# Optimization experiments

Measured on AMD Instinct MI355X. Metric: run time of the kernel, lower is better.

## Reference

```python
import jax, jax.numpy as jnp
import numpy as np

DIM = 512
HEADS = 8
DIM_HEAD = 64
INNER = HEADS * DIM_HEAD  # 512
B, N = 32, 512
LN_EPS = 1e-5


def setup_inputs() -> dict:
    key = jax.random.key(0)
    ks = jax.random.split(key, 8)
    inp = {
        "q": jax.random.normal(ks[0], (B, N, DIM), jnp.float32),
        "k": jax.random.normal(ks[1], (B, N, DIM), jnp.float32),
        "v": jax.random.normal(ks[2], (B, N, DIM), jnp.float32),
        "ln_w": jnp.ones((DIM,), jnp.float32),
        "ln_b": jnp.zeros((DIM,), jnp.float32),
        "W_in": jax.random.normal(ks[3], (DIM, INNER), jnp.float32) / np.sqrt(DIM),
        "W_out": jax.random.normal(ks[4], (INNER, DIM), jnp.float32) / np.sqrt(INNER),
        "b_out": jnp.zeros((DIM,), jnp.float32),
        "cov_w_raw": jnp.float32(0.6),
        "var_w_raw": jnp.float32(0.2),
    }
    return inp


def _project(x, ln_w, ln_b, W_in):
    # LayerNorm(dim) -> Linear(dim, inner, bias=False) -> 'b n (h d) -> h b n d'
    mu = jnp.mean(x, axis=-1, keepdims=True)
    var = jnp.var(x, axis=-1, keepdims=True)  # biased, as in nn.LayerNorm
    xn = (x - mu) / jnp.sqrt(var + LN_EPS) * ln_w + ln_b
    f = xn @ W_in  # [B, N, inner]
    Bq, Nq, _ = f.shape
    f = f.reshape(Bq, Nq, HEADS, DIM_HEAD)
    return jnp.transpose(f, (2, 0, 1, 3))  # [h, B, N, d]


def reference(q, k, v, ln_w, ln_b, W_in, W_out, b_out, cov_w_raw, var_w_raw):
    f_q = _project(q, ln_w, ln_b, W_in)  # [h, B, N, d]
    f_k = _project(k, ln_w, ln_b, W_in)
    f_v = _project(v, ln_w, ln_b, W_in)

    d = f_q.shape[-1]

    # cosine similarity: (q . k) / (||q|| ||k||)
    dots = jnp.einsum('hbnd,hbmd->hbnm', f_q, f_k)
    qn = jnp.linalg.norm(f_q, axis=-1)  # [h, B, N]
    kn = jnp.linalg.norm(f_k, axis=-1)  # [h, B, M]
    cosine_sim = dots / (qn[..., :, None] * kn[..., None, :])

    # basic covariance component: centered dot / d
    qc = f_q - jnp.mean(f_q, axis=-1, keepdims=True)
    kc = f_k - jnp.mean(f_k, axis=-1, keepdims=True)
    cov_component = jnp.einsum('hbnd,hbmd->hbnm', qc, kc) / d

    # variance component: outer product of per-token variances (unbiased) / d
    q_var = jnp.var(f_q, axis=-1, ddof=1)  # [h, B, N]
    k_var = jnp.var(f_k, axis=-1, ddof=1)  # [h, B, M]
    var_component = (q_var[..., :, None] * k_var[..., None, :]) / d

    cov_w = jax.nn.sigmoid(cov_w_raw)
    var_w = jax.nn.sigmoid(var_w_raw)
    cos_w = 1.0 - cov_w - var_w

    scores = cos_w * cosine_sim + cov_w * cov_component + var_w * var_component
    out = jnp.einsum('hbnm,hbmd->hbnd', scores, f_v)  # no softmax in cosine variant

    # 'h b n d -> b n (h d)'
    out = jnp.transpose(out, (1, 2, 0, 3)).reshape(out.shape[1], out.shape[2], INNER)
    return out @ W_out + b_out
```

## Files before the change

kernel.cpp:

```cpp
#include <hip/hip_runtime.h>
#include <stdint.h>

using u16 = unsigned short;
using u32 = unsigned int;
using bf16x8 = __bf16 __attribute__((ext_vector_type(8)));
using f32x4  = float __attribute__((ext_vector_type(4)));

__device__ __forceinline__ float bflo(u32 u){ return __uint_as_float(u << 16); }
__device__ __forceinline__ float bfhi(u32 u){ return __uint_as_float(u & 0xffff0000u); }
__device__ __forceinline__ u16 f2bf(float f){
  u32 u = __float_as_uint(f);
  u += 0x7fffu + ((u >> 16) & 1u);
  return (u16)(u >> 16);
}
__device__ __forceinline__ u32 pk2(float a, float b){
  return (u32)f2bf(a) | ((u32)f2bf(b) << 16);
}
__device__ __forceinline__ void gload16(const void* g, void* l){
  __builtin_amdgcn_global_load_lds(
      (const __attribute__((address_space(1))) void*)(uintptr_t)(g),
      (__attribute__((address_space(3))) void*)(uintptr_t)(l), 16, 0, 0);
}

__global__ __launch_bounds__(256) void prepcast_k(
    const float* __restrict__ q, const float* __restrict__ k, const float* __restrict__ v,
    const float* __restrict__ lnw, const float* __restrict__ lnb,
    u16* __restrict__ xnq, u16* __restrict__ xnk, u16* __restrict__ xnv,
    const float* __restrict__ Win, const float* __restrict__ Wout,
    u16* __restrict__ WinT, u16* __restrict__ WoutT){
  __shared__ float tile[32][33];
  if (blockIdx.x >= 12288){
    int bi = blockIdx.x - 12288;
    int bz = bi >> 8; bi &= 255;
    int bx = bi & 15, by = bi >> 4;
    const float* src = bz ? Wout : Win;
    u16* dst = bz ? WoutT : WinT;
    int tx = threadIdx.x & 31, ty = threadIdx.x >> 5;
    int c0 = bx * 32, r0 = by * 32;
#pragma unroll
    for (int i = 0; i < 4; ++i)
      tile[ty + i*8][tx] = src[(size_t)(r0 + ty + i*8)*512 + c0 + tx];
    __syncthreads();
#pragma unroll
    for (int i = 0; i < 4; ++i)
      dst[(size_t)(c0 + ty + i*8)*512 + r0 + tx] = f2bf(tile[tx][ty + i*8]);
    return;
  }
  int row = blockIdx.x * 4 + (threadIdx.x >> 6);
  int l = threadIdx.x & 63;
  const float* x = (row < 16384) ? q : (row < 32768) ? k : v;
  u16* xo = (row < 16384) ? xnq : (row < 32768) ? xnk : xnv;
  int r = row & 16383;
  const float* rp = x + (size_t)r * 512 + l*8;
  float4 a = *(const float4*)rp, c = *(const float4*)(rp + 4);
  float sum = ((a.x+a.y)+(a.z+a.w)) + ((c.x+c.y)+(c.z+c.w));
  float ss  = ((a.x*a.x+a.y*a.y)+(a.z*a.z+a.w*a.w)) + ((c.x*c.x+c.y*c.y)+(c.z*c.z+c.w*c.w));
#pragma unroll
  for (int off = 32; off; off >>= 1){
    sum += __shfl_xor(sum, off);
    ss  += __shfl_xor(ss,  off);
  }
  float mu = sum * (1.f/512.f);
  float rs = rsqrtf(ss * (1.f/512.f) - mu*mu + 1e-5f);
  float4 w0 = *(const float4*)(lnw + l*8), w1 = *(const float4*)(lnw + l*8 + 4);
  float4 b0 = *(const float4*)(lnb + l*8), b1 = *(const float4*)(lnb + l*8 + 4);
  uint4 pk;
  pk.x = pk2((a.x-mu)*rs*w0.x + b0.x, (a.y-mu)*rs*w0.y + b0.y);
  pk.y = pk2((a.z-mu)*rs*w0.z + b0.z, (a.w-mu)*rs*w0.w + b0.w);
  pk.z = pk2((c.x-mu)*rs*w1.x + b1.x, (c.y-mu)*rs*w1.y + b1.y);
  pk.w = pk2((c.z-mu)*rs*w1.z + b1.z, (c.w-mu)*rs*w1.w + b1.w);
  *(uint4*)((char*)xo + (size_t)r*1024 + l*16) = pk;
}

template<int MAP, int FSTAT>
__device__ __forceinline__ void gemm_body(
    const u16* __restrict__ A, const u16* __restrict__ B,
    u16* __restrict__ C, float* __restrict__ stat, int ldC, int bid,
    char* sA, char* sB){
  const int t = threadIdx.x, w = t >> 6, l = t & 63;
  const int wr = w >> 1, wc = w & 1;
  const int lr = l & 15, lg = l >> 4;
  int bx, by;
  if (MAP == 0){ bx = bid & 127; by = bid >> 7; }
  else { int j = bid >> 3; bx = j & 3; by = (bid & 7) + 8*(j >> 2); }
  const int row0 = bx * 128, col0 = by * 128;
  f32x4 acc[4][4] = {};

  const int sc = t >> 3, k8 = t & 7;
  const int sso = (k8*16) ^ ((sc & 7) << 4);
  const char* Ap = (const char*)A + ((size_t)(row0 + sc) << 10) + sso;
  const char* Bp = (const char*)B + ((size_t)(col0 + sc) << 10) + sso;

  for (int kt = 0; kt < 8; ++kt){
    __syncthreads();
#pragma unroll
    for (int ii = 0; ii < 4; ++ii){
      gload16(Ap + (size_t)ii*32768 + kt*128, sA + ii*4096 + w*1024);
      gload16(Bp + (size_t)ii*32768 + kt*128, sB + ii*4096 + w*1024);
    }
    __syncthreads();
#pragma unroll
    for (int kk = 0; kk < 2; ++kk){
      bf16x8 af[4], bfg[4];
#pragma unroll
      for (int m = 0; m < 4; ++m){
        int r = wr*64 + m*16 + lr;
        af[m] = *(const bf16x8*)(sA + r*128 + ((kk*64 + lg*16) ^ ((r & 7) << 4)));
      }
#pragma unroll
      for (int n = 0; n < 4; ++n){
        int r = wc*64 + n*16 + lr;
        bfg[n] = *(const bf16x8*)(sB + r*128 + ((kk*64 + lg*16) ^ ((r & 7) << 4)));
      }
#pragma unroll
      for (int m = 0; m < 4; ++m)
#pragma unroll
        for (int n = 0; n < 4; ++n)
          acc[m][n] = __builtin_amdgcn_mfma_f32_16x16x32_bf16(af[m], bfg[n], acc[m][n], 0, 0, 0);
    }
  }
  float cs[4] = {}, cs2[4] = {};
#pragma unroll
  for (int m = 0; m < 4; ++m){
#pragma unroll
    for (int q = 0; q < 4; ++q){
      int ri = wr*64 + m*16 + lg*4 + q;
      float fv[4];
#pragma unroll
      for (int n = 0; n < 4; ++n){
        int ci = wc*64 + n*16 + lr;
        fv[n] = acc[m][n][q];
        C[(size_t)(row0 + ri)*ldC + (col0 + ci)] = f2bf(fv[n]);
        if (FSTAT == 2){ cs[n] += fv[n]; cs2[n] += fv[n]*fv[n]; }
      }
      if (FSTAT == 1){
        float s  = (fv[0]+fv[1]) + (fv[2]+fv[3]);
        float s2 = (fv[0]*fv[0]+fv[1]*fv[1]) + (fv[2]*fv[2]+fv[3]*fv[3]);
#pragma unroll
        for (int off = 1; off < 16; off <<= 1){ s += __shfl_xor(s, off); s2 += __shfl_xor(s2, off); }
        if (lr == 0){
          int head = (col0 >> 6) + wc;
          *(float2*)(stat + ((size_t)(row0 + ri)*8 + head)*2) = make_float2(s, s2);
        }
      }
    }
  }
  if (FSTAT == 2){
    int head = (row0 >> 6) + wr;
#pragma unroll
    for (int n = 0; n < 4; ++n){
      float s = cs[n], s2 = cs2[n];
      s += __shfl_xor(s, 16); s2 += __shfl_xor(s2, 16);
      s += __shfl_xor(s, 32); s2 += __shfl_xor(s2, 32);
      if (lg == 0){
        int tok = col0 + wc*64 + n*16 + lr;
        *(float2*)(stat + ((size_t)tok*8 + head)*2) = make_float2(s, s2);
      }
    }
  }
}

__global__ __launch_bounds__(256) void proj_k(
    const u16* __restrict__ xnq, const u16* __restrict__ xnk, const u16* __restrict__ xnv,
    const u16* __restrict__ Wt,
    u16* __restrict__ fq, u16* __restrict__ kT, u16* __restrict__ vT,
    float* __restrict__ qstat, float* __restrict__ kstat){
  __shared__ __align__(16) char sA[16384];
  __shared__ __align__(16) char sB[16384];
  int bid = blockIdx.x;
  if (bid < 512)
    gemm_body<0,1>(xnq, Wt, fq, qstat, 512, bid, sA, sB);
  else if (bid < 1024)
    gemm_body<1,2>(Wt, xnk, kT, kstat, 16384, bid - 512, sA, sB);
  else
    gemm_body<1,0>(Wt, xnv, vT, nullptr, 16384, bid - 1024, sA, sB);
}

__global__ __launch_bounds__(256) void outgemm_k(
    const u16* __restrict__ A, const u16* __restrict__ B,
    float* __restrict__ Cf, const float* __restrict__ bias){
  __shared__ __align__(16) char sA[16384];
  __shared__ __align__(16) char sB[16384];
  const int t = threadIdx.x, w = t >> 6, l = t & 63;
  const int wr = w >> 1, wc = w & 1;
  const int lr = l & 15, lg = l >> 4;
  const int row0 = blockIdx.x * 128, col0 = blockIdx.y * 128;
  f32x4 acc[4][4] = {};

  const int sc = t >> 3, k8 = t & 7;
  const int sso = (k8*16) ^ ((sc & 7) << 4);
  const char* Ap = (const char*)A + ((size_t)(row0 + sc) << 10) + sso;
  const char* Bp = (const char*)B + ((size_t)(col0 + sc) << 10) + sso;

  for (int kt = 0; kt < 8; ++kt){
    __syncthreads();
#pragma unroll
    for (int ii = 0; ii < 4; ++ii){
      gload16(Ap + (size_t)ii*32768 + kt*128, sA + ii*4096 + w*1024);
      gload16(Bp + (size_t)ii*32768 + kt*128, sB + ii*4096 + w*1024);
    }
    __syncthreads();
#pragma unroll
    for (int kk = 0; kk < 2; ++kk){
      bf16x8 af[4], bfg[4];
#pragma unroll
      for (int m = 0; m < 4; ++m){
        int r = wr*64 + m*16 + lr;
        af[m] = *(const bf16x8*)(sA + r*128 + ((kk*64 + lg*16) ^ ((r & 7) << 4)));
      }
#pragma unroll
      for (int n = 0; n < 4; ++n){
        int r = wc*64 + n*16 + lr;
        bfg[n] = *(const bf16x8*)(sB + r*128 + ((kk*64 + lg*16) ^ ((r & 7) << 4)));
      }
#pragma unroll
      for (int m = 0; m < 4; ++m)
#pragma unroll
        for (int n = 0; n < 4; ++n)
          acc[m][n] = __builtin_amdgcn_mfma_f32_16x16x32_bf16(af[m], bfg[n], acc[m][n], 0, 0, 0);
    }
  }
#pragma unroll
  for (int m = 0; m < 4; ++m){
#pragma unroll
    for (int q = 0; q < 4; ++q){
      int r = row0 + wr*64 + m*16 + lg*4 + q;
#pragma unroll
      for (int n = 0; n < 4; ++n){
        int cc = col0 + wc*64 + n*16 + lr;
        Cf[(size_t)r*512 + cc] = acc[m][n][q] + bias[cc];
      }
    }
  }
}

__global__ __launch_bounds__(512) void attn_k(
    const u16* __restrict__ fq, const u16* __restrict__ kT, const u16* __restrict__ vT,
    const float* __restrict__ qstat, const float* __restrict__ kstat,
    u16* __restrict__ ao,
    const float* __restrict__ cwr, const float* __restrict__ vwr){
  __shared__ __align__(16) char smem[131072 + 1664*4];
  float* sStat = (float*)(smem + 131072);
  float* sS1 = sStat + 1536;
  float* sS2 = sStat + 1600;

  const int t = threadIdx.x, w = t >> 6, l = t & 63;
  const int lr = l & 15, lg = l >> 4;
  const int h = blockIdx.x & 7, b = blockIdx.x >> 3;

  float cwv = 1.f/(1.f + __expf(-*cwr));
  float vwv = 1.f/(1.f + __expf(-*vwr));
  float cosw = 1.f - cwv - vwv;

  const char* kTb = (const char*)kT + (size_t)h*64*32768 + (size_t)b*1024;
  const char* vTb = (const char*)vT + (size_t)h*64*32768 + (size_t)b*1024;
#pragma unroll
  for (int ii = 0; ii < 8; ++ii){
    int c = ii*512 + t, d = c >> 6, u = c & 63;
    int so = d*32768 + ((u ^ (d & 7)) << 4);
    gload16(kTb + so, smem + ii*8192 + w*1024);
    gload16(vTb + so, smem + 65536 + ii*8192 + w*1024);
  }
  {
    float2 ksr = *(const float2*)(kstat + ((size_t)(b*512 + t)*8 + h)*2);
    float mk = ksr.x * (1.f/64.f);
    sStat[t]        = rsqrtf(ksr.y);
    sStat[512 + t]  = mk;
    sStat[1024 + t] = (ksr.y - 64.f*mk*mk) * (1.f/63.f);
  }
  __syncthreads();

  const int jt = (w >> 1), itp = (w & 1);
  f32x4 m2acc[2] = {}, m1acc[2] = {};
  {
    const int j = jt*16 + lr;
#pragma unroll
    for (int ks = 0; ks < 16; ++ks){
      int u = ks*4 + lg;
      bf16x8 af = *(const bf16x8*)(smem + 65536 + j*1024 + ((u ^ (j & 7)) << 4));
#pragma unroll
      for (int tt = 0; tt < 2; ++tt){
        int i = (itp*2 + tt)*16 + lr;
        bf16x8 bf = *(const bf16x8*)(smem + i*1024 + ((u ^ (i & 7)) << 4));
        m2acc[tt] = __builtin_amdgcn_mfma_f32_16x16x32_bf16(af, bf, m2acc[tt], 0, 0, 0);
      }
    }
  }
  {
    int j = t >> 3, g = t & 7;
    float p1 = 0.f, p2 = 0.f;
#pragma unroll
    for (int uu = 0; uu < 8; ++uu){
      int ut = g*8 + uu;
      uint4 uv = *(const uint4*)(smem + 65536 + j*1024 + ((ut ^ (j & 7)) << 4));
      int m0 = ut*8;
      float4 mk0 = *(const float4*)(sStat + 512 + m0);
      float4 mk1 = *(const float4*)(sStat + 512 + m0 + 4);
      float4 kv0 = *(const float4*)(sStat + 1024 + m0);
      float4 kv1 = *(const float4*)(sStat + 1024 + m0 + 4);
      float v0=bflo(uv.x),v1=bfhi(uv.x),v2=bflo(uv.y),v3=bfhi(uv.y);
      float v4=bflo(uv.z),v5=bfhi(uv.z),v6=bflo(uv.w),v7=bfhi(uv.w);
      p1 += v0*mk0.x + v1*mk0.y + v2*mk0.z + v3*mk0.w
          + v4*mk1.x + v5*mk1.y + v6*mk1.z + v7*mk1.w;
      p2 += v0*kv0.x + v1*kv0.y + v2*kv0.z + v3*kv0.w
          + v4*kv1.x + v5*kv1.y + v6*kv1.z + v7*kv1.w;
    }
#pragma unroll
    for (int off = 1; off < 8; off <<= 1){ p1 += __shfl_xor(p1, off); p2 += __shfl_xor(p2, off); }
    if (g == 0){ sS1[j] = p1; sS2[j] = p2; }
  }
  __syncthreads();

#pragma unroll
  for (int ii = 0; ii < 32; ++ii){
    int wd = ii*512 + t;
    int d = wd >> 8, o = wd & 255, ud = o >> 2, p = o & 3;
    int m0 = ((ud ^ (d & 7)) << 3) + p*2;
    u32 uv = *(u32*)(smem + wd*4);
    *(u32*)(smem + wd*4) = pk2(bflo(uv)*sStat[m0], bfhi(uv)*sStat[m0+1]);
  }
  __syncthreads();

  {
    const int j = jt*16 + lr;
#pragma unroll
    for (int ks = 0; ks < 16; ++ks){
      int u = ks*4 + lg;
      bf16x8 af = *(const bf16x8*)(smem + 65536 + j*1024 + ((u ^ (j & 7)) << 4));
#pragma unroll
      for (int tt = 0; tt < 2; ++tt){
        int i = (itp*2 + tt)*16 + lr;
        bf16x8 bf = *(const bf16x8*)(smem + i*1024 + ((u ^ (i & 7)) << 4));
        m1acc[tt] = __builtin_amdgcn_mfma_f32_16x16x32_bf16(af, bf, m1acc[tt], 0, 0, 0);
      }
    }
  }
  __syncthreads();

#pragma unroll
  for (int tt = 0; tt < 2; ++tt){
#pragma unroll
    for (int q = 0; q < 4; ++q){
      int j = jt*16 + lg*4 + q;
      int i = (itp*2 + tt)*16 + lr;
      int bo = j*128 + (((i >> 3) ^ (j & 7)) << 4) + (i & 7)*2;
      *(u16*)(smem + bo)        = f2bf(m1acc[tt][q]);
      *(u16*)(smem + 8192 + bo) = f2bf(m2acc[tt][q]);
    }
  }
  const char* fqb = (const char*)fq + (size_t)b*524288 + h*128;
#pragma unroll
  for (int ii = 0; ii < 8; ++ii){
    int c = ii*512 + t, n = c >> 3, u = c & 7;
    gload16(fqb + n*1024 + ((u ^ (n & 7)) << 4), smem + 65536 + ii*8192 + w*1024);
  }
  __syncthreads();

  float s1v[4], s2v[4];
#pragma unroll
  for (int nt = 0; nt < 4; ++nt){ s1v[nt] = sS1[nt*16 + lr]; s2v[nt] = sS2[nt*16 + lr]; }
  const float Bc = cwv * (1.f/64.f);

#pragma unroll
  for (int mt = 0; mt < 4; ++mt){
    f32x4 a1[4] = {}, a2[4] = {};
    const int n = w*64 + mt*16 + lr;
#pragma unroll
    for (int kk = 0; kk < 2; ++kk){
      int u = kk*4 + lg;
      bf16x8 af = *(const bf16x8*)(smem + 65536 + n*128 + ((u ^ (n & 7)) << 4));
#pragma unroll
      for (int nt = 0; nt < 4; ++nt){
        int j = nt*16 + lr;
        bf16x8 b1 = *(const bf16x8*)(smem + j*128 + ((u ^ (j & 7)) << 4));
        bf16x8 b2 = *(const bf16x8*)(smem + 8192 + j*128 + ((u ^ (j & 7)) << 4));
        a1[nt] = __builtin_amdgcn_mfma_f32_16x16x32_bf16(af, b1, a1[nt], 0, 0, 0);
        a2[nt] = __builtin_amdgcn_mfma_f32_16x16x32_bf16(af, b2, a2[nt], 0, 0, 0);
      }
    }
#pragma unroll
    for (int q = 0; q < 4; ++q){
      int nr = w*64 + mt*16 + lg*4 + q;
      float2 qs = *(const float2*)(qstat + ((size_t)(b*512 + nr)*8 + h)*2);
      float mq = qs.x * (1.f/64.f);
      float An = cosw * rsqrtf(qs.y);
      float Cn = -cwv * mq;
      float En = vwv * (1.f/64.f) * ((qs.y - 64.f*mq*mq) * (1.f/63.f));
      char* op = (char*)ao + ((size_t)(b*512 + nr)*512 + h*64)*2;
#pragma unroll
      for (int nt = 0; nt < 4; ++nt){
        float ov = An*a1[nt][q] + Bc*a2[nt][q] + Cn*s1v[nt] + En*s2v[nt];
        *(u16*)(op + (nt*16 + lr)*2) = f2bf(ov);
      }
    }
  }
}

extern "C" void kernel_launch(void* const* d_in, const int* in_sizes, int n_in,
                              void* d_out, int out_size, void* d_ws, size_t ws_size,
                              hipStream_t stream){
  const float* q    = (const float*)d_in[0];
  const float* k    = (const float*)d_in[1];
  const float* v    = (const float*)d_in[2];
  const float* lnw  = (const float*)d_in[3];
  const float* lnb  = (const float*)d_in[4];
  const float* Win  = (const float*)d_in[5];
  const float* Wout = (const float*)d_in[6];
  const float* bout = (const float*)d_in[7];
  const float* cwr  = (const float*)d_in[8];
  const float* vwr  = (const float*)d_in[9];

  char* ws = (char*)d_ws;
  const size_t FB = (size_t)16384 * 512 * 2;
  u16* xnq = (u16*)(ws);
  u16* xnk = (u16*)(ws + FB);
  u16* xnv = (u16*)(ws + 2*FB);
  u16* fq  = (u16*)(ws + 3*FB);
  u16* kT  = (u16*)(ws + 4*FB);
  u16* vT  = (u16*)(ws + 5*FB);
  u16* ao  = (u16*)(ws + 6*FB);
  u16* WinT  = (u16*)(ws + 7*FB);
  u16* WoutT = (u16*)(ws + 7*FB + 524288);
  float* qstat = (float*)d_out;
  float* kstat = qstat + 262144;

  prepcast_k<<<12800, 256, 0, stream>>>(q, k, v, lnw, lnb, xnq, xnk, xnv,
                                        Win, Wout, WinT, WoutT);

  proj_k<<<1536, 256, 0, stream>>>(xnq, xnk, xnv, WinT, fq, kT, vT, qstat, kstat);

  attn_k<<<256, 512, 0, stream>>>(fq, kT, vT, qstat, kstat, ao, cwr, vwr);

  outgemm_k<<<dim3(128,4), 256, 0, stream>>>(ao, WoutT, (float*)d_out, bout);
}
```

Baseline: 101.7 us.

## Multi-stage pipeline GEMM K-loop, share body with out-projection, two rows per LN wave

The GEMM body now uses a four-buffer ring of 64-wide K slices in LDS. Loads are issued three stages ahead and gated by explicit vmcnt waits with one barrier per step, replacing the load-then-compute loop that had two barriers per step. The output projection reuses the same templated body with an fp32+bias epilogue. The LayerNorm/cast kernel processes two rows per wave to halve the block count. LDS use grows to 64KB per block, which may lower occupancy, and the LDS swizzle layout changes.

```diff
diff --git a/kernel.cpp b/kernel.cpp
--- a/kernel.cpp
+++ b/kernel.cpp
@@ -29,8 +29,8 @@
     const float* __restrict__ Win, const float* __restrict__ Wout,
     u16* __restrict__ WinT, u16* __restrict__ WoutT){
   __shared__ float tile[32][33];
-  if (blockIdx.x >= 12288){
-    int bi = blockIdx.x - 12288;
+  if (blockIdx.x >= 6144){
+    int bi = blockIdx.x - 6144;
     int bz = bi >> 8; bi &= 255;
     int bx = bi & 15, by = bi >> 4;
     const float* src = bz ? Wout : Win;
@@ -46,91 +46,114 @@
       dst[(size_t)(c0 + ty + i*8)*512 + r0 + tx] = f2bf(tile[tx][ty + i*8]);
     return;
   }
-  int row = blockIdx.x * 4 + (threadIdx.x >> 6);
-  int l = threadIdx.x & 63;
-  const float* x = (row < 16384) ? q : (row < 32768) ? k : v;
-  u16* xo = (row < 16384) ? xnq : (row < 32768) ? xnk : xnv;
-  int r = row & 16383;
-  const float* rp = x + (size_t)r * 512 + l*8;
-  float4 a = *(const float4*)rp, c = *(const float4*)(rp + 4);
-  float sum = ((a.x+a.y)+(a.z+a.w)) + ((c.x+c.y)+(c.z+c.w));
-  float ss  = ((a.x*a.x+a.y*a.y)+(a.z*a.z+a.w*a.w)) + ((c.x*c.x+c.y*c.y)+(c.z*c.z+c.w*c.w));
+  const int w = threadIdx.x >> 6, l = threadIdx.x & 63;
+  int rb = blockIdx.x * 8;
+  int r1 = rb + w, r2 = rb + 4 + w;
+  const float* x = (r1 < 16384) ? q : (r1 < 32768) ? k : v;
+  u16* xo = (r1 < 16384) ? xnq : (r1 < 32768) ? xnk : xnv;
+  int a1 = r1 & 16383, a2 = r2 & 16383;
+  const float* p1 = x + (size_t)a1*512 + l*8;
+  const float* p2 = x + (size_t)a2*512 + l*8;
+  float4 a = *(const float4*)p1, c = *(const float4*)(p1 + 4);
+  float4 d = *(const float4*)p2, e = *(const float4*)(p2 + 4);
+  float s1 = ((a.x+a.y)+(a.z+a.w)) + ((c.x+c.y)+(c.z+c.w));
+  float q1 = ((a.x*a.x+a.y*a.y)+(a.z*a.z+a.w*a.w)) + ((c.x*c.x+c.y*c.y)+(c.z*c.z+c.w*c.w));
+  float s2 = ((d.x+d.y)+(d.z+d.w)) + ((e.x+e.y)+(e.z+e.w));
+  float q2 = ((d.x*d.x+d.y*d.y)+(d.z*d.z+d.w*d.w)) + ((e.x*e.x+e.y*e.y)+(e.z*e.z+e.w*e.w));
 #pragma unroll
   for (int off = 32; off; off >>= 1){
-    sum += __shfl_xor(sum, off);
-    ss  += __shfl_xor(ss,  off);
-  }
-  float mu = sum * (1.f/512.f);
-  float rs = rsqrtf(ss * (1.f/512.f) - mu*mu + 1e-5f);
+    s1 += __shfl_xor(s1, off); q1 += __shfl_xor(q1, off);
+    s2 += __shfl_xor(s2, off); q2 += __shfl_xor(q2, off);
+  }
+  float mu1 = s1 * (1.f/512.f);
+  float rs1 = rsqrtf(q1 * (1.f/512.f) - mu1*mu1 + 1e-5f);
+  float mu2 = s2 * (1.f/512.f);
+  float rs2 = rsqrtf(q2 * (1.f/512.f) - mu2*mu2 + 1e-5f);
   float4 w0 = *(const float4*)(lnw + l*8), w1 = *(const float4*)(lnw + l*8 + 4);
   float4 b0 = *(const float4*)(lnb + l*8), b1 = *(const float4*)(lnb + l*8 + 4);
   uint4 pk;
-  pk.x = pk2((a.x-mu)*rs*w0.x + b0.x, (a.y-mu)*rs*w0.y + b0.y);
-  pk.y = pk2((a.z-mu)*rs*w0.z + b0.z, (a.w-mu)*rs*w0.w + b0.w);
-  pk.z = pk2((c.x-mu)*rs*w1.x + b1.x, (c.y-mu)*rs*w1.y + b1.y);
-  pk.w = pk2((c.z-mu)*rs*w1.z + b1.z, (c.w-mu)*rs*w1.w + b1.w);
-  *(uint4*)((char*)xo + (size_t)r*1024 + l*16) = pk;
-}
-
-template<int MAP, int FSTAT>
+  pk.x = pk2((a.x-mu1)*rs1*w0.x + b0.x, (a.y-mu1)*rs1*w0.y + b0.y);
+  pk.y = pk2((a.z-mu1)*rs1*w0.z + b0.z, (a.w-mu1)*rs1*w0.w + b0.w);
+  pk.z = pk2((c.x-mu1)*rs1*w1.x + b1.x, (c.y-mu1)*rs1*w1.y + b1.y);
+  pk.w = pk2((c.z-mu1)*rs1*w1.z + b1.z, (c.w-mu1)*rs1*w1.w + b1.w);
+  *(uint4*)((char*)xo + (size_t)a1*1024 + l*16) = pk;
+  pk.x = pk2((d.x-mu2)*rs2*w0.x + b0.x, (d.y-mu2)*rs2*w0.y + b0.y);
+  pk.y = pk2((d.z-mu2)*rs2*w0.z + b0.z, (d.w-mu2)*rs2*w0.w + b0.w);
+  pk.z = pk2((e.x-mu2)*rs2*w1.x + b1.x, (e.y-mu2)*rs2*w1.y + b1.y);
+  pk.w = pk2((e.z-mu2)*rs2*w1.z + b1.z, (e.w-mu2)*rs2*w1.w + b1.w);
+  *(uint4*)((char*)xo + (size_t)a2*1024 + l*16) = pk;
+}
+
+template<int MAP, int FSTAT, int F32OUT>
 __device__ __forceinline__ void gemm_body(
     const u16* __restrict__ A, const u16* __restrict__ B,
-    u16* __restrict__ C, float* __restrict__ stat, int ldC, int bid,
-    char* sA, char* sB){
+    u16* __restrict__ C, float* __restrict__ Cf,
+    float* __restrict__ stat, const float* __restrict__ bias,
+    int ldC, int bid, char* sM){
   const int t = threadIdx.x, w = t >> 6, l = t & 63;
   const int wr = w >> 1, wc = w & 1;
   const int lr = l & 15, lg = l >> 4;
   int bx, by;
   if (MAP == 0){ bx = bid & 127; by = bid >> 7; }
   else { int j = bid >> 3; bx = j & 3; by = (bid & 7) + 8*(j >> 2); }
-  const int row0 = bx * 128, col0 = by * 128;
+  const int row0 = bx*128, col0 = by*128;
+
+  const int spr = t >> 3, se = (t & 7) ^ (spr & 7);
+  const int srow = spr*2 + (se >> 2), sk16 = se & 3;
+  const char* Ap0 = (const char*)A + ((size_t)(row0 + srow) << 10) + sk16*16;
+  const char* Bp0 = (const char*)B + ((size_t)(col0 + srow) << 10) + sk16*16;
+  const int ldst = w*1024 + l*16;
+
+  const int qf = ((((lr & 1) << 2) | lg) ^ ((lr >> 1) & 7)) * 16;
+  const int afb = wr*4096 + (lr >> 1)*128 + qf;
+  const int bfb = wc*4096 + (lr >> 1)*128 + qf;
+
   f32x4 acc[4][4] = {};
 
-  const int sc = t >> 3, k8 = t & 7;
-  const int sso = (k8*16) ^ ((sc & 7) << 4);
-  const char* Ap = (const char*)A + ((size_t)(row0 + sc) << 10) + sso;
-  const char* Bp = (const char*)B + ((size_t)(col0 + sc) << 10) + sso;
-
-  for (int kt = 0; kt < 8; ++kt){
-    __syncthreads();
-#pragma unroll
-    for (int ii = 0; ii < 4; ++ii){
-      gload16(Ap + (size_t)ii*32768 + kt*128, sA + ii*4096 + w*1024);
-      gload16(Bp + (size_t)ii*32768 + kt*128, sB + ii*4096 + w*1024);
-    }
-    __syncthreads();
-#pragma unroll
-    for (int kk = 0; kk < 2; ++kk){
-      bf16x8 af[4], bfg[4];
-#pragma unroll
-      for (int m = 0; m < 4; ++m){
-        int r = wr*64 + m*16 + lr;
-        af[m] = *(const bf16x8*)(sA + r*128 + ((kk*64 + lg*16) ^ ((r & 7) << 4)));
-      }
-#pragma unroll
-      for (int n = 0; n < 4; ++n){
-        int r = wc*64 + n*16 + lr;
-        bfg[n] = *(const bf16x8*)(sB + r*128 + ((kk*64 + lg*16) ^ ((r & 7) << 4)));
-      }
-#pragma unroll
-      for (int m = 0; m < 4; ++m)
-#pragma unroll
-        for (int n = 0; n < 4; ++n)
-          acc[m][n] = __builtin_amdgcn_mfma_f32_16x16x32_bf16(af[m], bfg[n], acc[m][n], 0, 0, 0);
-    }
-  }
+  auto STAGE = [&](int kt, int buf){
+    char* d = sM + buf*16384;
+    gload16(Ap0 + kt*64,         d + ldst);
+    gload16(Ap0 + 65536 + kt*64, d + 4096 + ldst);
+    gload16(Bp0 + kt*64,         d + 8192 + ldst);
+    gload16(Bp0 + 65536 + kt*64, d + 12288 + ldst);
+  };
+
+  STAGE(0, 0); STAGE(1, 1); STAGE(2, 2);
+#pragma unroll
+  for (int kt = 0; kt < 16; ++kt){
+    if (kt < 14)       asm volatile("s_waitcnt vmcnt(8)" ::: "memory");
+    else if (kt == 14) asm volatile("s_waitcnt vmcnt(4)" ::: "memory");
+    else               asm volatile("s_waitcnt vmcnt(0)" ::: "memory");
+    __builtin_amdgcn_s_barrier();
+    __builtin_amdgcn_sched_barrier(0);
+    if (kt < 13) STAGE(kt + 3, (kt + 3) & 3);
+    const char* aR = sM + (kt & 3)*16384;
+    const char* bR = aR + 8192;
+    bf16x8 af[4], bfg[4];
+#pragma unroll
+    for (int m = 0; m < 4; ++m) af[m]  = *(const bf16x8*)(aR + afb + m*1024);
+#pragma unroll
+    for (int n = 0; n < 4; ++n) bfg[n] = *(const bf16x8*)(bR + bfb + n*1024);
+#pragma unroll
+    for (int m = 0; m < 4; ++m)
+#pragma unroll
+      for (int n = 0; n < 4; ++n)
+        acc[m][n] = __builtin_amdgcn_mfma_f32_16x16x32_bf16(af[m], bfg[n], acc[m][n], 0, 0, 0);
+  }
+
   float cs[4] = {}, cs2[4] = {};
 #pragma unroll
   for (int m = 0; m < 4; ++m){
 #pragma unroll
-    for (int q = 0; q < 4; ++q){
-      int ri = wr*64 + m*16 + lg*4 + q;
+    for (int qq = 0; qq < 4; ++qq){
+      int ri = wr*64 + m*16 + lg*4 + qq;
       float fv[4];
 #pragma unroll
       for (int n = 0; n < 4; ++n){
         int ci = wc*64 + n*16 + lr;
-        fv[n] = acc[m][n][q];
-        C[(size_t)(row0 + ri)*ldC + (col0 + ci)] = f2bf(fv[n]);
+        fv[n] = acc[m][n][qq];
+        if (F32OUT) Cf[(size_t)(row0 + ri)*ldC + (col0 + ci)] = fv[n] + bias[col0 + ci];
+        else        C [(size_t)(row0 + ri)*ldC + (col0 + ci)] = f2bf(fv[n]);
         if (FSTAT == 2){ cs[n] += fv[n]; cs2[n] += fv[n]*fv[n]; }
       }
       if (FSTAT == 1){
@@ -165,73 +188,21 @@
     const u16* __restrict__ Wt,
     u16* __restrict__ fq, u16* __restrict__ kT, u16* __restrict__ vT,
     float* __restrict__ qstat, float* __restrict__ kstat){
-  __shared__ __align__(16) char sA[16384];
-  __shared__ __align__(16) char sB[16384];
+  __shared__ __align__(16) char sM[65536];
   int bid = blockIdx.x;
   if (bid < 512)
-    gemm_body<0,1>(xnq, Wt, fq, qstat, 512, bid, sA, sB);
+    gemm_body<0,1,0>(xnq, Wt, fq, nullptr, qstat, nullptr, 512, bid, sM);
   else if (bid < 1024)
-    gemm_body<1,2>(Wt, xnk, kT, kstat, 16384, bid - 512, sA, sB);
+    gemm_body<1,2,0>(Wt, xnk, kT, nullptr, kstat, nullptr, 16384, bid - 512, sM);
   else
-    gemm_body<1,0>(Wt, xnv, vT, nullptr, 16384, bid - 1024, sA, sB);
+    gemm_body<1,0,0>(Wt, xnv, vT, nullptr, nullptr, nullptr, 16384, bid - 1024, sM);
 }
 
 __global__ __launch_bounds__(256) void outgemm_k(
     const u16* __restrict__ A, const u16* __restrict__ B,
     float* __restrict__ Cf, const float* __restrict__ bias){
-  __shared__ __align__(16) char sA[16384];
-  __shared__ __align__(16) char sB[16384];
-  const int t = threadIdx.x, w = t >> 6, l = t & 63;
-  const int wr = w >> 1, wc = w & 1;
-  const int lr = l & 15, lg = l >> 4;
-  const int row0 = blockIdx.x * 128, col0 = blockIdx.y * 128;
-  f32x4 acc[4][4] = {};
-
-  const int sc = t >> 3, k8 = t & 7;
-  const int sso = (k8*16) ^ ((sc & 7) << 4);
-  const char* Ap = (const char*)A + ((size_t)(row0 + sc) << 10) + sso;
-  const char* Bp = (const char*)B + ((size_t)(col0 + sc) << 10) + sso;
-
-  for (int kt = 0; kt < 8; ++kt){
-    __syncthreads();
-#pragma unroll
-    for (int ii = 0; ii < 4; ++ii){
-      gload16(Ap + (size_t)ii*32768 + kt*128, sA + ii*4096 + w*1024);
-      gload16(Bp + (size_t)ii*32768 + kt*128, sB + ii*4096 + w*1024);
-    }
-    __syncthreads();
-#pragma unroll
-    for (int kk = 0; kk < 2; ++kk){
-      bf16x8 af[4], bfg[4];
-#pragma unroll
-      for (int m = 0; m < 4; ++m){
-        int r = wr*64 + m*16 + lr;
-        af[m] = *(const bf16x8*)(sA + r*128 + ((kk*64 + lg*16) ^ ((r & 7) << 4)));
-      }
-#pragma unroll
-      for (int n = 0; n < 4; ++n){
-        int r = wc*64 + n*16 + lr;
-        bfg[n] = *(const bf16x8*)(sB + r*128 + ((kk*64 + lg*16) ^ ((r & 7) << 4)));
-      }
-#pragma unroll
-      for (int m = 0; m < 4; ++m)
-#pragma unroll
-        for (int n = 0; n < 4; ++n)
-          acc[m][n] = __builtin_amdgcn_mfma_f32_16x16x32_bf16(af[m], bfg[n], acc[m][n], 0, 0, 0);
-    }
-  }
-#pragma unroll
-  for (int m = 0; m < 4; ++m){
-#pragma unroll
-    for (int q = 0; q < 4; ++q){
-      int r = row0 + wr*64 + m*16 + lg*4 + q;
-#pragma unroll
-      for (int n = 0; n < 4; ++n){
-        int cc = col0 + wc*64 + n*16 + lr;
-        Cf[(size_t)r*512 + cc] = acc[m][n][q] + bias[cc];
-      }
-    }
-  }
+  __shared__ __align__(16) char sM[65536];
+  gemm_body<0,0,1>(A, B, nullptr, Cf, nullptr, bias, 512, blockIdx.x, sM);
 }
 
 __global__ __launch_bounds__(512) void attn_k(
@@ -424,12 +395,12 @@
   float* qstat = (float*)d_out;
   float* kstat = qstat + 262144;
 
-  prepcast_k<<<12800, 256, 0, stream>>>(q, k, v, lnw, lnb, xnq, xnk, xnv,
-                                        Win, Wout, WinT, WoutT);
+  prepcast_k<<<6656, 256, 0, stream>>>(q, k, v, lnw, lnb, xnq, xnk, xnv,
+                                       Win, Wout, WinT, WoutT);
 
   proj_k<<<1536, 256, 0, stream>>>(xnq, xnk, xnv, WinT, fq, kT, vT, qstat, kstat);
 
   attn_k<<<256, 512, 0, stream>>>(fq, kT, vT, qstat, kstat, ao, cwr, vwr);
 
-  outgemm_k<<<dim3(128,4), 256, 0, stream>>>(ao, WoutT, (float*)d_out, bout);
-}
+  outgemm_k<<<512, 256, 0, stream>>>(ao, WoutT, (float*)d_out, bout);
+}
```

New measurement: 102.7 us. Within noise of the previous version (+1.0%).
